# Optimization experiments

Measured on AMD Instinct MI355X. Metric: run time of the kernel, lower is better.

The kernel has to match this reference:

```python
import jax, jax.numpy as jnp
import numpy as np


def setup_inputs() -> dict:
    key = jax.random.key(0)
    k1, k2 = jax.random.split(key)
    # bilateral grid: [N, grid_h, grid_w, grid_d, C]
    grid = jax.random.normal(k1, (4, 16, 16, 8, 12), dtype=jnp.float32)
    # guide map in [0, 1]: [N, H, W]
    guide = jax.random.uniform(k2, (4, 1024, 1024), dtype=jnp.float32)
    return {"grid": grid, "guide": guide}


def reference(grid, guide):
    """HDRNet bilateral_slice: per-pixel trilinear interpolation into the
    bilateral grid, with z coordinate given by the guide map.

    grid:  [N, gh, gw, gd, C]
    guide: [N, H, W] in [0, 1]
    out:   [N, H, W, C]
    """
    N, gh, gw, gd, C = grid.shape
    _, H, W = guide.shape

    # continuous grid coordinates (pixel centers)
    gx = (jnp.arange(W, dtype=guide.dtype) + 0.5) * (gw / W)   # [W]
    gy = (jnp.arange(H, dtype=guide.dtype) + 0.5) * (gh / H)   # [H]
    gz = guide * gd                                            # [N, H, W]

    fx = jnp.floor(gx - 0.5)
    fy = jnp.floor(gy - 0.5)
    fz = jnp.floor(gz - 0.5)

    batch = jnp.arange(N)[:, None, None]                       # [N, 1, 1]
    out = jnp.zeros((N, H, W, C), dtype=grid.dtype)

    # 8 trilinear corners (2 taps per axis, tent weights, clamped indices)
    for i in (0, 1):
        xx = fx + i
        wx = jnp.maximum(1.0 - jnp.abs(xx + 0.5 - gx), 0.0)    # [W]
        cx = jnp.clip(xx, 0, gw - 1).astype(jnp.int32)
        for j in (0, 1):
            yy = fy + j
            wy = jnp.maximum(1.0 - jnp.abs(yy + 0.5 - gy), 0.0)  # [H]
            cy = jnp.clip(yy, 0, gh - 1).astype(jnp.int32)
            for k in (0, 1):
                zz = fz + k
                wz = jnp.maximum(1.0 - jnp.abs(zz + 0.5 - gz), 0.0)  # [N,H,W]
                cz = jnp.clip(zz, 0, gd - 1).astype(jnp.int32)
                # gather corner values: [N, H, W, C]
                vals = grid[batch, cy[None, :, None], cx[None, None, :], cz]
                w = (wy[None, :, None] * wx[None, None, :] * wz)[..., None]
                out = out + w * vals
    return out
```

## Files before the change

### kernel.cpp

```cpp
#include <hip/hip_runtime.h>


#define GH 16
#define GW 16
#define GD 8
#define NC 12
#define IMH 1024
#define IMW 1024
#define NBATCH 4
#define ROW_FLOATS (GW * GD * NC)
#define CELL_DW   (GD * NC)
#define Z_DW      (NC)

typedef float f32x4 __attribute__((ext_vector_type(4)));

__device__ __forceinline__ void fma4(f32x4& a, float w, const f32x4& v) {
    a = a + w * v;
}

__global__ __launch_bounds__(256) void bilateral_slice_kernel(
    const float* __restrict__ grid,
    const float* __restrict__ guide,
    float* __restrict__ out)
{
    __shared__ float rowlds[2 * ROW_FLOATS];

    const int t = threadIdx.x;
    const int idx = blockIdx.x * 256 + t;
    const int x = idx & (IMW - 1);
    const int y = (idx >> 10) & (IMH - 1);
    const int n = idx >> 20;

    const float gy = (y + 0.5f) * ((float)GH / (float)IMH);
    const float fy = floorf(gy - 0.5f);
    const int fyi = (int)fy;
    const int cy0 = min(max(fyi, 0), GH - 1);
    const int cy1 = min(max(fyi + 1, 0), GH - 1);
    float wy[2];
    wy[0] = fmaxf(1.0f - fabsf(fy + 0.5f - gy), 0.0f);
    wy[1] = fmaxf(1.0f - fabsf(fy + 1.5f - gy), 0.0f);

    const float* gbase = grid + (size_t)n * (GH * ROW_FLOATS);
    const f32x4* src0 = (const f32x4*)(gbase + cy0 * ROW_FLOATS);
    const f32x4* src1 = (const f32x4*)(gbase + cy1 * ROW_FLOATS);
    f32x4* dst = (f32x4*)rowlds;
#pragma unroll
    for (int s = 0; s < 3; ++s) {
        const int f = s * 256 + t;
        const int rs = (f >= 384) ? 1 : 0;
        const f32x4* src = rs ? src1 : src0;
        dst[f] = src[f - rs * 384];
    }

    const float gx = (x + 0.5f) * ((float)GW / (float)IMW);
    const float gz = guide[idx] * (float)GD;

    const float fx = floorf(gx - 0.5f);
    const float fz = floorf(gz - 0.5f);

    float wx[2], wz[2];
    int cx[2], cz[2];
#pragma unroll
    for (int i = 0; i < 2; ++i) {
        const float xx = fx + (float)i;
        const float zz = fz + (float)i;
        wx[i] = fmaxf(1.0f - fabsf(xx + 0.5f - gx), 0.0f);
        wz[i] = fmaxf(1.0f - fabsf(zz + 0.5f - gz), 0.0f);
        cx[i] = min(max((int)fx + i, 0), GW - 1);
        cz[i] = min(max((int)fz + i, 0), GD - 1);
    }

    __syncthreads();

    f32x4 a0 = (f32x4)0.f;
    f32x4 a1 = (f32x4)0.f;
    f32x4 a2 = (f32x4)0.f;

#pragma unroll
    for (int j = 0; j < 2; ++j) {
#pragma unroll
        for (int i = 0; i < 2; ++i) {
            const float wxy = wy[j] * wx[i];
            const int cellbase = j * ROW_FLOATS + cx[i] * CELL_DW;
#pragma unroll
            for (int k = 0; k < 2; ++k) {
                const float w = wxy * wz[k];
                const f32x4* g4 = (const f32x4*)&rowlds[cellbase + cz[k] * Z_DW];
                const f32x4 v0 = g4[0];
                const f32x4 v1 = g4[1];
                const f32x4 v2 = g4[2];
                fma4(a0, w, v0);
                fma4(a1, w, v1);
                fma4(a2, w, v2);
            }
        }
    }

    f32x4* o = (f32x4*)(out + (size_t)idx * NC);
    __builtin_nontemporal_store(a0, o + 0);
    __builtin_nontemporal_store(a1, o + 1);
    __builtin_nontemporal_store(a2, o + 2);
}

extern "C" void kernel_launch(void* const* d_in, const int* in_sizes, int n_in,
                              void* d_out, int out_size, void* d_ws, size_t ws_size,
                              hipStream_t stream) {
    const float* grid  = (const float*)d_in[0];
    const float* guide = (const float*)d_in[1];
    float* out = (float*)d_out;

    const int total_pixels = NBATCH * IMH * IMW;
    const int block = 256;
    const int nblocks = total_pixels / block;

    bilateral_slice_kernel<<<nblocks, block, 0, stream>>>(grid, guide, out);
}
```

Baseline: 269.5 us.

## Pre-blend y rows in LDS and write output with coalesced per-quarter stores

The two grid rows are blended by the y weights while staging into shared memory, so each output needs only 4 bilinear taps in x and z instead of 8 trilinear taps. The output loop is also remapped so each thread writes one float4 lane of consecutive output elements, which makes the global stores fully coalesced instead of three strided stores per pixel. Each thread now recomputes x and z weights and reloads the guide value for every quarter-pixel it handles. The nontemporal store hint is dropped.

```diff
diff --git a/kernel.cpp b/kernel.cpp
--- a/kernel.cpp
+++ b/kernel.cpp
@@ -14,92 +14,84 @@
 
 typedef float f32x4 __attribute__((ext_vector_type(4)));
 
-__device__ __forceinline__ void fma4(f32x4& a, float w, const f32x4& v) {
-    a = a + w * v;
-}
-
 __global__ __launch_bounds__(256) void bilateral_slice_kernel(
     const float* __restrict__ grid,
     const float* __restrict__ guide,
     float* __restrict__ out)
 {
-    __shared__ float rowlds[2 * ROW_FLOATS];
+    __shared__ float yrow[ROW_FLOATS];
 
     const int t = threadIdx.x;
-    const int idx = blockIdx.x * 256 + t;
-    const int x = idx & (IMW - 1);
-    const int y = (idx >> 10) & (IMH - 1);
-    const int n = idx >> 20;
+    const int b = blockIdx.x;
+    const int P0 = b * 256;
+    const int y = (b >> 2) & (IMH - 1);
+    const int n = b >> 12;
+    const int base_x = (b & 3) * 256;
 
     const float gy = (y + 0.5f) * ((float)GH / (float)IMH);
     const float fy = floorf(gy - 0.5f);
     const int fyi = (int)fy;
     const int cy0 = min(max(fyi, 0), GH - 1);
     const int cy1 = min(max(fyi + 1, 0), GH - 1);
-    float wy[2];
-    wy[0] = fmaxf(1.0f - fabsf(fy + 0.5f - gy), 0.0f);
-    wy[1] = fmaxf(1.0f - fabsf(fy + 1.5f - gy), 0.0f);
+    const float wy0 = fmaxf(1.0f - fabsf(fy + 0.5f - gy), 0.0f);
+    const float wy1 = fmaxf(1.0f - fabsf(fy + 1.5f - gy), 0.0f);
 
     const float* gbase = grid + (size_t)n * (GH * ROW_FLOATS);
-    const f32x4* src0 = (const f32x4*)(gbase + cy0 * ROW_FLOATS);
-    const f32x4* src1 = (const f32x4*)(gbase + cy1 * ROW_FLOATS);
-    f32x4* dst = (f32x4*)rowlds;
+    const f32x4* row0 = (const f32x4*)(gbase + cy0 * ROW_FLOATS);
+    const f32x4* row1 = (const f32x4*)(gbase + cy1 * ROW_FLOATS);
+    f32x4* Y4 = (f32x4*)yrow;
+    {
+        const f32x4 r0 = row0[t];
+        const f32x4 r1 = row1[t];
+        Y4[t] = wy0 * r0 + wy1 * r1;
+        if (t < 128) {
+            const f32x4 r0b = row0[256 + t];
+            const f32x4 r1b = row1[256 + t];
+            Y4[256 + t] = wy0 * r0b + wy1 * r1b;
+        }
+    }
+    __syncthreads();
+
+    f32x4* __restrict__ out4 = (f32x4*)out + (size_t)b * 768;
+
 #pragma unroll
     for (int s = 0; s < 3; ++s) {
-        const int f = s * 256 + t;
-        const int rs = (f >= 384) ? 1 : 0;
-        const f32x4* src = rs ? src1 : src0;
-        dst[f] = src[f - rs * 384];
+        const int e = s * 256 + t;
+        const int p = e / 3;
+        const int part = e - 3 * p;
+
+        const int x = base_x + p;
+        const float gx = (x + 0.5f) * ((float)GW / (float)IMW);
+        const float fx = floorf(gx - 0.5f);
+        const float wx0 = fmaxf(1.0f - fabsf(fx + 0.5f - gx), 0.0f);
+        const float wx1 = fmaxf(1.0f - fabsf(fx + 1.5f - gx), 0.0f);
+        const int cx0 = min(max((int)fx, 0), GW - 1);
+        const int cx1 = min(max((int)fx + 1, 0), GW - 1);
+
+        const float gz = guide[P0 + p] * (float)GD;
+        const float fz = floorf(gz - 0.5f);
+        const float wz0 = fmaxf(1.0f - fabsf(fz + 0.5f - gz), 0.0f);
+        const float wz1 = fmaxf(1.0f - fabsf(fz + 1.5f - gz), 0.0f);
+        const int cz0 = min(max((int)fz, 0), GD - 1);
+        const int cz1 = min(max((int)fz + 1, 0), GD - 1);
+
+        const int b00 = cx0 * CELL_DW + cz0 * Z_DW + part * 4;
+        const int b01 = cx0 * CELL_DW + cz1 * Z_DW + part * 4;
+        const int b10 = cx1 * CELL_DW + cz0 * Z_DW + part * 4;
+        const int b11 = cx1 * CELL_DW + cz1 * Z_DW + part * 4;
+
+        const f32x4 v00 = *(const f32x4*)&yrow[b00];
+        const f32x4 v01 = *(const f32x4*)&yrow[b01];
+        const f32x4 v10 = *(const f32x4*)&yrow[b10];
+        const f32x4 v11 = *(const f32x4*)&yrow[b11];
+
+        f32x4 acc = (wx0 * wz0) * v00;
+        acc += (wx0 * wz1) * v01;
+        acc += (wx1 * wz0) * v10;
+        acc += (wx1 * wz1) * v11;
+
+        out4[e] = acc;
     }
-
-    const float gx = (x + 0.5f) * ((float)GW / (float)IMW);
-    const float gz = guide[idx] * (float)GD;
-
-    const float fx = floorf(gx - 0.5f);
-    const float fz = floorf(gz - 0.5f);
-
-    float wx[2], wz[2];
-    int cx[2], cz[2];
-#pragma unroll
-    for (int i = 0; i < 2; ++i) {
-        const float xx = fx + (float)i;
-        const float zz = fz + (float)i;
-        wx[i] = fmaxf(1.0f - fabsf(xx + 0.5f - gx), 0.0f);
-        wz[i] = fmaxf(1.0f - fabsf(zz + 0.5f - gz), 0.0f);
-        cx[i] = min(max((int)fx + i, 0), GW - 1);
-        cz[i] = min(max((int)fz + i, 0), GD - 1);
-    }
-
-    __syncthreads();
-
-    f32x4 a0 = (f32x4)0.f;
-    f32x4 a1 = (f32x4)0.f;
-    f32x4 a2 = (f32x4)0.f;
-
-#pragma unroll
-    for (int j = 0; j < 2; ++j) {
-#pragma unroll
-        for (int i = 0; i < 2; ++i) {
-            const float wxy = wy[j] * wx[i];
-            const int cellbase = j * ROW_FLOATS + cx[i] * CELL_DW;
-#pragma unroll
-            for (int k = 0; k < 2; ++k) {
-                const float w = wxy * wz[k];
-                const f32x4* g4 = (const f32x4*)&rowlds[cellbase + cz[k] * Z_DW];
-                const f32x4 v0 = g4[0];
-                const f32x4 v1 = g4[1];
-                const f32x4 v2 = g4[2];
-                fma4(a0, w, v0);
-                fma4(a1, w, v1);
-                fma4(a2, w, v2);
-            }
-        }
-    }
-
-    f32x4* o = (f32x4*)(out + (size_t)idx * NC);
-    __builtin_nontemporal_store(a0, o + 0);
-    __builtin_nontemporal_store(a1, o + 1);
-    __builtin_nontemporal_store(a2, o + 2);
 }
 
 extern "C" void kernel_launch(void* const* d_in, const int* in_sizes, int n_in,
```

New measurement: 221.7 us. 17.8% less time.
